# Performance work log

Measured on AMD Instinct MI355X. Metric: run time of the kernel, lower is better.

The kernel has to match this reference:

```python
import jax, jax.numpy as jnp
import numpy as np

EPS = 1e-5
GROUPS = 8
NUM_HEADS = 8


def setup_inputs() -> dict:
    key = jax.random.key(0)
    ks = jax.random.split(key, 6)
    C = 512
    s = 1.0 / np.sqrt(C)
    return {
        "x": jax.random.normal(ks[0], (8, C, 32, 32), dtype=jnp.float32),
        "gn_w": jnp.ones((C,), jnp.float32),
        "gn_b": jnp.zeros((C,), jnp.float32),
        "wq": jax.random.normal(ks[1], (C, C), jnp.float32) * s,
        "bq": jnp.zeros((C,), jnp.float32),
        "wk": jax.random.normal(ks[2], (C, C), jnp.float32) * s,
        "bk": jnp.zeros((C,), jnp.float32),
        "wv": jax.random.normal(ks[3], (C, C), jnp.float32) * s,
        "bv": jnp.zeros((C,), jnp.float32),
        "wp": jax.random.normal(ks[4], (C, C), jnp.float32) * s,
        "bp": jnp.zeros((C,), jnp.float32),
    }


def _group_norm(x, w, b):
    # x: [B, C, H, W]; normalize per group over (C//G, H, W)
    B, C, H, W = x.shape
    xg = x.reshape(B, GROUPS, -1)
    mean = xg.mean(axis=-1, keepdims=True)
    var = xg.var(axis=-1, keepdims=True)
    xn = ((xg - mean) * jax.lax.rsqrt(var + EPS)).reshape(B, C, H, W)
    return xn * w[None, :, None, None] + b[None, :, None, None]


def reference(x, gn_w, gn_b, wq, bq, wk, bk, wv, bv, wp, bp):
    B, C, H, W = x.shape
    n_heads = NUM_HEADS
    d = C // n_heads
    scale = 1.0 / np.sqrt(d)

    x_flat = x.reshape(B, C, H * W).transpose(0, 2, 1)       # [B, S, C]
    xn = _group_norm(x, gn_w, gn_b).reshape(B, C, H * W).transpose(0, 2, 1)

    # torch Linear: y = x @ W.T + b
    q = (xn @ wq.T + bq).reshape(B, H * W, n_heads, d)        # [B, S, h, d]
    k = (xn @ wk.T + bk).reshape(B, H * W, n_heads, d)
    v = (xn @ wv.T + bv).reshape(B, H * W, n_heads, d)

    attn = jnp.einsum("bnhd,bmhd->bhnm", q, k) * scale       # [B, h, S, S]
    attn = jax.nn.softmax(attn, axis=-1)
    out = jnp.einsum("bhnm,bmhd->bnhd", attn, v).reshape(B, H * W, C)
    out = out @ wp.T + bp
    out = out + x_flat
    return out.transpose(0, 2, 1).reshape(B, C, H, W)
```

## Files before the change

### kernel.cpp

```cpp
#include <hip/hip_runtime.h>
#include <stdint.h>

typedef unsigned short u16;
using bf16x8 = __attribute__((ext_vector_type(8))) short;
using f32x4  = __attribute__((ext_vector_type(4))) float;
using f32x16 = __attribute__((ext_vector_type(16))) float;
typedef unsigned int uv2 __attribute__((ext_vector_type(2)));

#define EPS_GN 1e-5f
#define SCL 0.18033688011112042f

__device__ __forceinline__ u16 f2bf(float f) {
  union { float f; uint32_t u; } x; x.f = f;
  uint32_t r = x.u + 0x7FFFu + ((x.u >> 16) & 1u);
  return (u16)(r >> 16);
}

__device__ __forceinline__ void gload_lds16(const void* g, void* l) {
  __builtin_amdgcn_global_load_lds(
      (const __attribute__((address_space(1))) unsigned int*)g,
      (__attribute__((address_space(3))) unsigned int*)l, 16, 0, 0);
}

__device__ __forceinline__ void fence_tile() {
  asm volatile("s_waitcnt vmcnt(0)" ::: "memory");
  __builtin_amdgcn_s_barrier();
  __builtin_amdgcn_sched_barrier(0);
}

__global__ __launch_bounds__(256) void prep(const float* __restrict__ x,
    float* __restrict__ part,
    const float4* __restrict__ wq, const float4* __restrict__ wk,
    const float4* __restrict__ wv, const float4* __restrict__ wp,
    const float* __restrict__ bq, const float* __restrict__ bk,
    const float* __restrict__ bv,
    u16* __restrict__ wqkv, u16* __restrict__ wpb, float* __restrict__ bqkv) {
  if (blockIdx.x < 512) {
    int bg = blockIdx.x >> 3, seg = blockIdx.x & 7;
    const float4* base = (const float4*)(x + (size_t)bg * 65536 + (size_t)seg * 8192);
    float s = 0.f, s2 = 0.f;
    for (int i = threadIdx.x; i < 2048; i += 256) {
      float4 v = base[i];
      s  += v.x + v.y + v.z + v.w;
      s2 += v.x*v.x + v.y*v.y + v.z*v.z + v.w*v.w;
    }
    for (int m = 1; m < 64; m <<= 1) { s += __shfl_xor(s, m); s2 += __shfl_xor(s2, m); }
    __shared__ float red[4][2];
    int wave = threadIdx.x >> 6;
    if ((threadIdx.x & 63) == 0) { red[wave][0] = s; red[wave][1] = s2; }
    __syncthreads();
    if (threadIdx.x == 0) {
      float a = 0.f, b = 0.f;
      for (int w = 0; w < 4; ++w) { a += red[w][0]; b += red[w][1]; }
      part[blockIdx.x * 2] = a; part[blockIdx.x * 2 + 1] = b;
    }
  } else {
    int i = (blockIdx.x - 512) * 256 + threadIdx.x;
    int seg = i >> 16, j = i & 65535;
    const float4* w = (seg == 0) ? wq : (seg == 1) ? wk : (seg == 2) ? wv : wp;
    u16* o = (seg < 3) ? (wqkv + seg * 262144) : wpb;
    float sc = (seg == 0) ? SCL : 1.f;
    float4 v = w[j];
    o[j*4+0] = f2bf(v.x*sc); o[j*4+1] = f2bf(v.y*sc);
    o[j*4+2] = f2bf(v.z*sc); o[j*4+3] = f2bf(v.w*sc);
    if (i < 1536) bqkv[i] = (i < 512) ? bq[i]*SCL : (i < 1024) ? bk[i-512] : bv[i-1024];
  }
}

__global__ __launch_bounds__(256) void gn_apply(const float* __restrict__ x,
    const float* __restrict__ part, const float* __restrict__ w,
    const float* __restrict__ bb, u16* __restrict__ xn) {
  __shared__ float t[32][33];
  int s0 = blockIdx.x * 32, c0 = blockIdx.y * 32, b = blockIdx.z;
  int g = c0 >> 6;
  float s = 0.f, s2 = 0.f;
  for (int q = 0; q < 8; ++q) {
    s  += part[((b*8+g)*8 + q)*2];
    s2 += part[((b*8+g)*8 + q)*2 + 1];
  }
  float mean = s * (1.f/65536.f);
  float rstd = rsqrtf(s2 * (1.f/65536.f) - mean*mean + EPS_GN);
  for (int i = 0; i < 4; ++i) {
    int c = c0 + threadIdx.y + i * 8;
    float v = x[((size_t)b*512 + c)*1024 + s0 + threadIdx.x];
    t[threadIdx.y + i*8][threadIdx.x] = (v - mean) * rstd * w[c] + bb[c];
  }
  __syncthreads();
  for (int i = 0; i < 4; ++i) {
    int sdx = s0 + threadIdx.y + i * 8;
    xn[((size_t)b*1024 + sdx)*512 + c0 + threadIdx.x] = f2bf(t[threadIdx.x][threadIdx.y + i*8]);
  }
}

__global__ __launch_bounds__(256) void qkv_gemm(const u16* __restrict__ X,
    const u16* __restrict__ W, const float* __restrict__ bias,
    u16* __restrict__ qb, u16* __restrict__ kP, u16* __restrict__ vP) {
  __shared__ __align__(16) u16 As[2*64*64];
  __shared__ __align__(16) u16 Bs[2*128*64];
  const int K = 512;
  int m0 = (blockIdx.x & 127) * 64, n0 = (blockIdx.x >> 7) * 128;
  int t = threadIdx.x, lane = t & 63, wave = t >> 6;
  int wm = wave >> 1, wn = wave & 1;
  int lr = lane & 15, lg = lane >> 4;
  f32x4 acc[2][4] = {};

  auto stage = [&](int k0, int bufi) {
    u16* Ab = As + bufi * 4096;
    u16* Bb = Bs + bufi * 8192;
#pragma unroll
    for (int c = 0; c < 2; ++c) {
      int chunk = wave * 2 + c;
      int e = chunk * 512 + lane * 8;
      int r = e >> 6, col = e & 63;
      int scol = col ^ ((r & 7) << 3);
      gload_lds16(X + (size_t)(m0 + r) * K + k0 + scol, (char*)Ab + chunk * 1024);
    }
#pragma unroll
    for (int c = 0; c < 4; ++c) {
      int chunk = wave * 4 + c;
      int e = chunk * 512 + lane * 8;
      int r = e >> 6, col = e & 63;
      int scol = col ^ ((r & 7) << 3);
      gload_lds16(W + (size_t)(n0 + r) * K + k0 + scol, (char*)Bb + chunk * 1024);
    }
  };

  stage(0, 0);
  fence_tile();
  int buf = 0;
  for (int k0 = 0; k0 < K; k0 += 64) {
    if (k0 + 64 < K) stage(k0 + 64, buf ^ 1);
    const char* Ab = (const char*)(As + buf * 4096);
    const char* Bb = (const char*)(Bs + buf * 8192);
    bf16x8 af[2][2], bfr[4][2];
#pragma unroll
    for (int kk = 0; kk < 2; ++kk) {
      int ca = kk * 64 + lg * 16;
#pragma unroll
      for (int i = 0; i < 2; ++i) {
        int ra = wm * 32 + i * 16 + lr;
        af[i][kk] = *(const bf16x8*)(Ab + ((ra * 128 + ca) ^ ((ra & 7) << 4)));
      }
#pragma unroll
      for (int j = 0; j < 4; ++j) {
        int rb = wn * 64 + j * 16 + lr;
        bfr[j][kk] = *(const bf16x8*)(Bb + ((rb * 128 + ca) ^ ((rb & 7) << 4)));
      }
    }
    __builtin_amdgcn_s_setprio(1);
#pragma unroll
    for (int kk = 0; kk < 2; ++kk)
#pragma unroll
      for (int i = 0; i < 2; ++i)
#pragma unroll
        for (int j = 0; j < 4; ++j)
          acc[i][j] = __builtin_amdgcn_mfma_f32_16x16x32_bf16(af[i][kk], bfr[j][kk], acc[i][j], 0, 0, 0);
    __builtin_amdgcn_s_setprio(0);
    fence_tile();
    buf ^= 1;
  }
  if (n0 < 512) {
    for (int i = 0; i < 2; ++i)
      for (int j = 0; j < 4; ++j) {
        int col = n0 + wn * 64 + j * 16 + lr;
        float bv = bias[col];
        int rowb = m0 + wm * 32 + i * 16 + lg * 4;
        for (int r = 0; r < 4; ++r)
          qb[(size_t)(rowb + r) * 512 + col] = f2bf(acc[i][j][r] + bv);
      }
  } else if (n0 < 1024) {
    for (int i = 0; i < 2; ++i)
      for (int j = 0; j < 4; ++j) {
        int col = n0 + wn * 64 + j * 16 + lr;
        float bv = bias[col];
        int colK = col - 512;
        int h = colK >> 6, dcol = colK & 63;
        int s = dcol >> 4, hi2 = (dcol >> 3) & 1, jj = dcol & 7;
        int rowb = m0 + wm * 32 + i * 16 + lg * 4;
        int bb2 = rowb >> 10, s_in = rowb & 1023;
        int tile = s_in >> 6, kvl = s_in & 63;
        int n2 = kvl >> 5, lq0 = kvl & 31;
        size_t base = ((size_t)(((h * 8 + bb2) * 16 + tile) * 8 + n2 * 4 + s)) * 512 + jj;
        for (int r = 0; r < 4; ++r)
          kP[base + (size_t)(hi2 * 32 + lq0 + r) * 8] = f2bf(acc[i][j][r] + bv);
      }
  } else {
    for (int i = 0; i < 2; ++i)
      for (int j = 0; j < 4; ++j) {
        int col = n0 + wn * 64 + j * 16 + lr;
        float bv = bias[col];
        int rowb = m0 + wm * 32 + i * 16 + lg * 4;
        int colV = col - 1024;
        int h  = colV >> 6, dl = colV & 63;
        int dt = dl >> 5,  lqv = dl & 31;
        int bb2 = rowb >> 10, s_in = rowb & 1023;
        int tile = s_in >> 6, kvl = s_in & 63;
        int cg = kvl >> 4, hiv = (kvl >> 3) & 1, j0 = kvl & 7;
        int ii = dt * 4 + cg, lv = hiv * 32 + lqv;
        size_t u16off = ((size_t)((h * 8 + bb2) * 16 + tile)) * 4096 + (ii * 64 + lv) * 8 + j0;
        unsigned p0, p1;
        float v0 = acc[i][j][0] + bv, v1 = acc[i][j][1] + bv;
        float v2 = acc[i][j][2] + bv, v3 = acc[i][j][3] + bv;
        asm("v_cvt_pk_bf16_f32 %0, %1, %2" : "=v"(p0) : "v"(v0), "v"(v1));
        asm("v_cvt_pk_bf16_f32 %0, %1, %2" : "=v"(p1) : "v"(v2), "v"(v3));
        uint2 pk; pk.x = p0; pk.y = p1;
        *(uint2*)(vP + u16off) = pk;
      }
  }
}

__global__ __launch_bounds__(256) void proj_gemm(const u16* __restrict__ Wt,
    const u16* __restrict__ X, const float* __restrict__ bias,
    const float* __restrict__ resid, float* __restrict__ Out) {
  __shared__ __align__(16) u16 As[2*128*64];
  __shared__ __align__(16) u16 Bs[2*64*64];
  const int K = 512;
  int m0 = blockIdx.x * 64, n0 = blockIdx.y * 128;
  int t = threadIdx.x, lane = t & 63, wave = t >> 6;
  int wm = wave >> 1, wn = wave & 1;
  int lr = lane & 15, lg = lane >> 4;
  f32x4 acc[4][2] = {};

  auto stage = [&](int k0, int bufi) {
    u16* Ab = As + bufi * 8192;
    u16* Bb = Bs + bufi * 4096;
#pragma unroll
    for (int c = 0; c < 4; ++c) {
      int chunk = wave * 4 + c;
      int e = chunk * 512 + lane * 8;
      int r = e >> 6, col = e & 63;
      int scol = col ^ ((r & 7) << 3);
      gload_lds16(Wt + (size_t)(n0 + r) * K + k0 + scol, (char*)Ab + chunk * 1024);
    }
#pragma unroll
    for (int c = 0; c < 2; ++c) {
      int chunk = wave * 2 + c;
      int e = chunk * 512 + lane * 8;
      int r = e >> 6, col = e & 63;
      int scol = col ^ ((r & 7) << 3);
      gload_lds16(X + (size_t)(m0 + r) * K + k0 + scol, (char*)Bb + chunk * 1024);
    }
  };

  stage(0, 0);
  fence_tile();
  int buf = 0;
  for (int k0 = 0; k0 < K; k0 += 64) {
    if (k0 + 64 < K) stage(k0 + 64, buf ^ 1);
    const char* Ab = (const char*)(As + buf * 8192);
    const char* Bb = (const char*)(Bs + buf * 4096);
    bf16x8 af[4][2], bfr[2][2];
#pragma unroll
    for (int kk = 0; kk < 2; ++kk) {
      int ca = kk * 64 + lg * 16;
#pragma unroll
      for (int i = 0; i < 4; ++i) {
        int ra = wm * 64 + i * 16 + lr;
        af[i][kk] = *(const bf16x8*)(Ab + ((ra * 128 + ca) ^ ((ra & 7) << 4)));
      }
#pragma unroll
      for (int j = 0; j < 2; ++j) {
        int rb = wn * 32 + j * 16 + lr;
        bfr[j][kk] = *(const bf16x8*)(Bb + ((rb * 128 + ca) ^ ((rb & 7) << 4)));
      }
    }
    __builtin_amdgcn_s_setprio(1);
#pragma unroll
    for (int kk = 0; kk < 2; ++kk)
#pragma unroll
      for (int i = 0; i < 4; ++i)
#pragma unroll
        for (int j = 0; j < 2; ++j)
          acc[i][j] = __builtin_amdgcn_mfma_f32_16x16x32_bf16(af[i][kk], bfr[j][kk], acc[i][j], 0, 0, 0);
    __builtin_amdgcn_s_setprio(0);
    fence_tile();
    buf ^= 1;
  }
  for (int i = 0; i < 4; ++i)
    for (int j = 0; j < 2; ++j) {
      int mcol = m0 + wn * 32 + j * 16 + lr;
      for (int r = 0; r < 4; ++r) {
        int nrow = n0 + wm * 64 + i * 16 + lg * 4 + r;
        float v = acc[i][j][r] + bias[nrow];
        size_t b = (size_t)(mcol >> 10); int s = mcol & 1023;
        size_t addr = (b * 512 + nrow) * 1024 + s;
        Out[addr] = v + resid[addr];
      }
    }
}

__global__ __launch_bounds__(512, 4) void attn_fwd(const u16* __restrict__ qb,
    const u16* __restrict__ kP, const u16* __restrict__ vP, u16* __restrict__ o) {
  __shared__ __align__(16) u16 smem[26624];
  int bh = blockIdx.x, qb_i = blockIdx.y;
  int b = bh >> 3, h = bh & 7;
  int t = threadIdx.x, lane = t & 63, wave = t >> 6;
  int half = wave >> 2, wq4 = wave & 3;
  int lq = lane & 31, hi = lane >> 5;
  int qrow0 = qb_i * 128 + wq4 * 32;
  const u16* qp = qb + (size_t)(b * 1024 + qrow0 + lq) * 512 + h * 64 + hi * 8;
  bf16x8 qf[4];
#pragma unroll
  for (int s = 0; s < 4; ++s) qf[s] = *(const bf16x8*)(qp + s * 16);
  float li = 0.f;
  f32x16 ot[2] = {};
  const u16* kb = kP + ((size_t)((h * 8 + b) * 16 + half * 8)) * 4096 + (size_t)lane * 8;
  const u16* vb = vP + ((size_t)((h * 8 + b) * 16 + half * 8)) * 4096 + (size_t)lane * 8;

  for (int ti = 0; ti < 8; ++ti) {
    bf16x8 kf[8];
#pragma unroll
    for (int f = 0; f < 8; ++f) kf[f] = *(const bf16x8*)(kb + ti * 4096 + f * 512);
    f32x16 st[2];
#pragma unroll
    for (int n2 = 0; n2 < 2; ++n2) {
      f32x16 z = {};
      __builtin_amdgcn_s_setprio(1);
#pragma unroll
      for (int s = 0; s < 4; ++s)
        z = __builtin_amdgcn_mfma_f32_32x32x16_bf16(kf[n2 * 4 + s], qf[s], z, 0, 0, 0);
      __builtin_amdgcn_s_setprio(0);
      st[n2] = z;
    }
    float sm[16];
#pragma unroll
    for (int r = 0; r < 16; ++r) {
      float e0 = __builtin_amdgcn_exp2f(st[0][r]);
      float e1 = __builtin_amdgcn_exp2f(st[1][r]);
      st[0][r] = e0; st[1][r] = e1;
      sm[r] = e0 + e1;
    }
#pragma unroll
    for (int s = 8; s > 0; s >>= 1)
#pragma unroll
      for (int r = 0; r < s; ++r) sm[r] += sm[r + s];
    li += sm[0] + __shfl_xor(sm[0], 32);
    bf16x8 fr[4];
#pragma unroll
    for (int n2 = 0; n2 < 2; ++n2) {
#pragma unroll
      for (int c = 0; c < 2; ++c) {
        unsigned W0, W1, W2, W3;
        asm("v_cvt_pk_bf16_f32 %0, %1, %2" : "=v"(W0) : "v"(st[n2][8*c+0]), "v"(st[n2][8*c+1]));
        asm("v_cvt_pk_bf16_f32 %0, %1, %2" : "=v"(W1) : "v"(st[n2][8*c+2]), "v"(st[n2][8*c+3]));
        asm("v_cvt_pk_bf16_f32 %0, %1, %2" : "=v"(W2) : "v"(st[n2][8*c+4]), "v"(st[n2][8*c+5]));
        asm("v_cvt_pk_bf16_f32 %0, %1, %2" : "=v"(W3) : "v"(st[n2][8*c+6]), "v"(st[n2][8*c+7]));
        uv2 r02 = __builtin_amdgcn_permlane32_swap(W0, W2, false, false);
        uv2 r13 = __builtin_amdgcn_permlane32_swap(W1, W3, false, false);
        union { unsigned u[4]; bf16x8 v; } f;
        f.u[0] = r02[0]; f.u[1] = r13[0]; f.u[2] = r02[1]; f.u[3] = r13[1];
        fr[n2 * 2 + c] = f.v;
      }
    }
    bf16x8 vr[8];
#pragma unroll
    for (int i = 0; i < 8; ++i) vr[i] = *(const bf16x8*)(vb + ti * 4096 + i * 512);
    __builtin_amdgcn_s_setprio(1);
#pragma unroll
    for (int cg = 0; cg < 4; ++cg)
#pragma unroll
      for (int dt = 0; dt < 2; ++dt)
        ot[dt] = __builtin_amdgcn_mfma_f32_32x32x16_bf16(vr[dt * 4 + cg], fr[cg], ot[dt], 0, 0, 0);
    __builtin_amdgcn_s_setprio(0);
  }
  float* cbuf = (float*)smem;
  float* wreg = cbuf + wq4 * 2176;
  if (half == 0) {
#pragma unroll
    for (int dt = 0; dt < 2; ++dt)
#pragma unroll
      for (int r = 0; r < 16; ++r)
        wreg[(dt * 16 + r) * 64 + lane] = ot[dt][r];
    wreg[2048 + lane] = li;
  }
  __syncthreads();
  if (half == 1) {
    float inv = 1.f / (wreg[2048 + lane] + li);
    u16* wb = smem + 18432 + wq4 * 2048;
#pragma unroll
    for (int dt = 0; dt < 2; ++dt)
#pragma unroll
      for (int g = 0; g < 4; ++g) {
        float v0 = (wreg[(dt*16 + 4*g+0)*64 + lane] + ot[dt][4*g+0]) * inv;
        float v1 = (wreg[(dt*16 + 4*g+1)*64 + lane] + ot[dt][4*g+1]) * inv;
        float v2 = (wreg[(dt*16 + 4*g+2)*64 + lane] + ot[dt][4*g+2]) * inv;
        float v3 = (wreg[(dt*16 + 4*g+3)*64 + lane] + ot[dt][4*g+3]) * inv;
        unsigned p0, p1;
        asm("v_cvt_pk_bf16_f32 %0, %1, %2" : "=v"(p0) : "v"(v0), "v"(v1));
        asm("v_cvt_pk_bf16_f32 %0, %1, %2" : "=v"(p1) : "v"(v2), "v"(v3));
        int ch = dt * 8 + 2 * g + hi;
        int pos = ch ^ ((lq & 7) << 1);
        uint2 wv; wv.x = p0; wv.y = p1;
        *(uint2*)((char*)wb + lq * 128 + pos * 8) = wv;
      }
    int q2 = lane >> 1, j0 = lane & 1;
#pragma unroll
    for (int jj = 0; jj < 4; ++jj) {
      int j = j0 + jj * 2;
      uint4 val = *(const uint4*)((const char*)wb + q2 * 128 + ((j ^ (q2 & 7)) << 4));
      *(uint4*)(o + (size_t)(b * 1024 + qrow0 + q2) * 512 + h * 64 + j * 8) = val;
    }
  }
}

extern "C" void kernel_launch(void* const* d_in, const int* in_sizes, int n_in,
                              void* d_out, int out_size, void* d_ws, size_t ws_size,
                              hipStream_t stream) {
  const float* x    = (const float*)d_in[0];
  const float* gn_w = (const float*)d_in[1];
  const float* gn_b = (const float*)d_in[2];
  const float* wq   = (const float*)d_in[3];
  const float* bq   = (const float*)d_in[4];
  const float* wk   = (const float*)d_in[5];
  const float* bk   = (const float*)d_in[6];
  const float* wv   = (const float*)d_in[7];
  const float* bv   = (const float*)d_in[8];
  const float* wp   = (const float*)d_in[9];
  const float* bp   = (const float*)d_in[10];

  char* ws = (char*)d_ws;
  float* part  = (float*)ws;
  float* bqkv  = (float*)(ws + 4096);
  u16* wqkv = (u16*)(ws + 16384);
  u16* wpb  = (u16*)(ws + 1589248);
  u16* xn   = (u16*)(ws + 2113536);
  u16* qb   = (u16*)(ws + 10502144);
  u16* kPb  = qb + 4194304;
  u16* vPb  = (u16*)(ws + 27279360);
  u16* attno = xn;

  prep<<<1536, 256, 0, stream>>>(x, part,
      (const float4*)wq, (const float4*)wk, (const float4*)wv, (const float4*)wp,
      bq, bk, bv, wqkv, wpb, bqkv);
  gn_apply<<<dim3(32, 16, 8), dim3(32, 8), 0, stream>>>(x, part, gn_w, gn_b, xn);
  qkv_gemm<<<1536, 256, 0, stream>>>(xn, wqkv, bqkv, qb, kPb, vPb);
  attn_fwd<<<dim3(64, 8), 512, 0, stream>>>(qb, kPb, vPb, attno);
  proj_gemm<<<dim3(128, 4), 256, 0, stream>>>(wpb, attno, bp, x, (float*)d_out);
}
```

Measured before the change: 74.34 us.

## Process two query row groups per wave in attention and double-buffer K fragments

Each wave now handles 64 query rows (two 32-row groups), so every K and V fragment loaded from memory feeds twice as many MFMAs, and the grid halves along the query axis. K fragments for the next tile are prefetched into a second register set while the current tile is computed, and the V loads are issued earlier to hide latency. This raises register pressure, so launch bounds drop to 2 blocks per SM. The cross-half combine is done once per query group with extra barriers. Fewer blocks and lower occupancy may leave CUs underused.

```diff
diff --git a/kernel.cpp b/kernel.cpp
--- a/kernel.cpp
+++ b/kernel.cpp
@@ -289,116 +289,175 @@
     }
 }
 
-__global__ __launch_bounds__(512, 4) void attn_fwd(const u16* __restrict__ qb,
+__global__ __launch_bounds__(512, 2) void attn_fwd(const u16* __restrict__ qbuf,
     const u16* __restrict__ kP, const u16* __restrict__ vP, u16* __restrict__ o) {
-  __shared__ __align__(16) u16 smem[26624];
-  int bh = blockIdx.x, qb_i = blockIdx.y;
+  __shared__ float comb[4][2112];
+  __shared__ __align__(16) u16 wbuf[4][2048];
+  int bh = blockIdx.x, qb2 = blockIdx.y;
   int b = bh >> 3, h = bh & 7;
   int t = threadIdx.x, lane = t & 63, wave = t >> 6;
   int half = wave >> 2, wq4 = wave & 3;
   int lq = lane & 31, hi = lane >> 5;
-  int qrow0 = qb_i * 128 + wq4 * 32;
-  const u16* qp = qb + (size_t)(b * 1024 + qrow0 + lq) * 512 + h * 64 + hi * 8;
-  bf16x8 qf[4];
-#pragma unroll
-  for (int s = 0; s < 4; ++s) qf[s] = *(const bf16x8*)(qp + s * 16);
-  float li = 0.f;
-  f32x16 ot[2] = {};
+  int qrow0 = qb2 * 256 + wq4 * 64;
+  bf16x8 qf[2][4];
+#pragma unroll
+  for (int g = 0; g < 2; ++g) {
+    const u16* qp = qbuf + (size_t)(b * 1024 + qrow0 + g * 32 + lq) * 512 + h * 64 + hi * 8;
+#pragma unroll
+    for (int s = 0; s < 4; ++s) qf[g][s] = *(const bf16x8*)(qp + s * 16);
+  }
+  float liA = 0.f, liB = 0.f;
+  f32x16 otA0 = {}, otA1 = {}, otB0 = {}, otB1 = {};
   const u16* kb = kP + ((size_t)((h * 8 + b) * 16 + half * 8)) * 4096 + (size_t)lane * 8;
   const u16* vb = vP + ((size_t)((h * 8 + b) * 16 + half * 8)) * 4096 + (size_t)lane * 8;
 
-  for (int ti = 0; ti < 8; ++ti) {
-    bf16x8 kf[8];
-#pragma unroll
-    for (int f = 0; f < 8; ++f) kf[f] = *(const bf16x8*)(kb + ti * 4096 + f * 512);
-    f32x16 st[2];
+  bf16x8 kfA[8], kfB[8];
+#pragma unroll
+  for (int f = 0; f < 8; ++f) kfA[f] = *(const bf16x8*)(kb + f * 512);
+
+  auto tile_body = [&](int ti, bf16x8 (&kf)[8], bf16x8 (&kn)[8]) {
+    f32x16 stA[2];
 #pragma unroll
     for (int n2 = 0; n2 < 2; ++n2) {
       f32x16 z = {};
       __builtin_amdgcn_s_setprio(1);
 #pragma unroll
       for (int s = 0; s < 4; ++s)
-        z = __builtin_amdgcn_mfma_f32_32x32x16_bf16(kf[n2 * 4 + s], qf[s], z, 0, 0, 0);
+        z = __builtin_amdgcn_mfma_f32_32x32x16_bf16(kf[n2 * 4 + s], qf[0][s], z, 0, 0, 0);
       __builtin_amdgcn_s_setprio(0);
-      st[n2] = z;
-    }
-    float sm[16];
+      stA[n2] = z;
+    }
+    bf16x8 vr[8];
+#pragma unroll
+    for (int i = 0; i < 8; ++i) vr[i] = *(const bf16x8*)(vb + ti * 4096 + i * 512);
+    f32x16 stB[2];
+#pragma unroll
+    for (int n2 = 0; n2 < 2; ++n2) {
+      f32x16 z = {};
+      __builtin_amdgcn_s_setprio(1);
+#pragma unroll
+      for (int s = 0; s < 4; ++s)
+        z = __builtin_amdgcn_mfma_f32_32x32x16_bf16(kf[n2 * 4 + s], qf[1][s], z, 0, 0, 0);
+      __builtin_amdgcn_s_setprio(0);
+      stB[n2] = z;
+    }
 #pragma unroll
     for (int r = 0; r < 16; ++r) {
-      float e0 = __builtin_amdgcn_exp2f(st[0][r]);
-      float e1 = __builtin_amdgcn_exp2f(st[1][r]);
-      st[0][r] = e0; st[1][r] = e1;
-      sm[r] = e0 + e1;
-    }
-#pragma unroll
-    for (int s = 8; s > 0; s >>= 1)
-#pragma unroll
-      for (int r = 0; r < s; ++r) sm[r] += sm[r + s];
-    li += sm[0] + __shfl_xor(sm[0], 32);
-    bf16x8 fr[4];
-#pragma unroll
-    for (int n2 = 0; n2 < 2; ++n2) {
+      stA[0][r] = __builtin_amdgcn_exp2f(stA[0][r]);
+      stA[1][r] = __builtin_amdgcn_exp2f(stA[1][r]);
+      stB[0][r] = __builtin_amdgcn_exp2f(stB[0][r]);
+      stB[1][r] = __builtin_amdgcn_exp2f(stB[1][r]);
+    }
+    bf16x8 frA[4], frB[4];
+#pragma unroll
+    for (int n2 = 0; n2 < 2; ++n2)
 #pragma unroll
       for (int c = 0; c < 2; ++c) {
         unsigned W0, W1, W2, W3;
-        asm("v_cvt_pk_bf16_f32 %0, %1, %2" : "=v"(W0) : "v"(st[n2][8*c+0]), "v"(st[n2][8*c+1]));
-        asm("v_cvt_pk_bf16_f32 %0, %1, %2" : "=v"(W1) : "v"(st[n2][8*c+2]), "v"(st[n2][8*c+3]));
-        asm("v_cvt_pk_bf16_f32 %0, %1, %2" : "=v"(W2) : "v"(st[n2][8*c+4]), "v"(st[n2][8*c+5]));
-        asm("v_cvt_pk_bf16_f32 %0, %1, %2" : "=v"(W3) : "v"(st[n2][8*c+6]), "v"(st[n2][8*c+7]));
+        asm("v_cvt_pk_bf16_f32 %0, %1, %2" : "=v"(W0) : "v"(stA[n2][8*c+0]), "v"(stA[n2][8*c+1]));
+        asm("v_cvt_pk_bf16_f32 %0, %1, %2" : "=v"(W1) : "v"(stA[n2][8*c+2]), "v"(stA[n2][8*c+3]));
+        asm("v_cvt_pk_bf16_f32 %0, %1, %2" : "=v"(W2) : "v"(stA[n2][8*c+4]), "v"(stA[n2][8*c+5]));
+        asm("v_cvt_pk_bf16_f32 %0, %1, %2" : "=v"(W3) : "v"(stA[n2][8*c+6]), "v"(stA[n2][8*c+7]));
         uv2 r02 = __builtin_amdgcn_permlane32_swap(W0, W2, false, false);
         uv2 r13 = __builtin_amdgcn_permlane32_swap(W1, W3, false, false);
         union { unsigned u[4]; bf16x8 v; } f;
         f.u[0] = r02[0]; f.u[1] = r13[0]; f.u[2] = r02[1]; f.u[3] = r13[1];
-        fr[n2 * 2 + c] = f.v;
-      }
-    }
-    bf16x8 vr[8];
-#pragma unroll
-    for (int i = 0; i < 8; ++i) vr[i] = *(const bf16x8*)(vb + ti * 4096 + i * 512);
+        frA[n2 * 2 + c] = f.v;
+      }
+#pragma unroll
+    for (int n2 = 0; n2 < 2; ++n2)
+#pragma unroll
+      for (int c = 0; c < 2; ++c) {
+        unsigned W0, W1, W2, W3;
+        asm("v_cvt_pk_bf16_f32 %0, %1, %2" : "=v"(W0) : "v"(stB[n2][8*c+0]), "v"(stB[n2][8*c+1]));
+        asm("v_cvt_pk_bf16_f32 %0, %1, %2" : "=v"(W1) : "v"(stB[n2][8*c+2]), "v"(stB[n2][8*c+3]));
+        asm("v_cvt_pk_bf16_f32 %0, %1, %2" : "=v"(W2) : "v"(stB[n2][8*c+4]), "v"(stB[n2][8*c+5]));
+        asm("v_cvt_pk_bf16_f32 %0, %1, %2" : "=v"(W3) : "v"(stB[n2][8*c+6]), "v"(stB[n2][8*c+7]));
+        uv2 r02 = __builtin_amdgcn_permlane32_swap(W0, W2, false, false);
+        uv2 r13 = __builtin_amdgcn_permlane32_swap(W1, W3, false, false);
+        union { unsigned u[4]; bf16x8 v; } f;
+        f.u[0] = r02[0]; f.u[1] = r13[0]; f.u[2] = r02[1]; f.u[3] = r13[1];
+        frB[n2 * 2 + c] = f.v;
+      }
+    if (ti < 7) {
+#pragma unroll
+      for (int f = 0; f < 8; ++f) kn[f] = *(const bf16x8*)(kb + (ti + 1) * 4096 + f * 512);
+    }
+#pragma unroll
+    for (int r = 0; r < 16; ++r) { stA[0][r] += stA[1][r]; stB[0][r] += stB[1][r]; }
+#pragma unroll
+    for (int s = 8; s > 0; s >>= 1)
+#pragma unroll
+      for (int r = 0; r < s; ++r) { stA[0][r] += stA[0][r + s]; stB[0][r] += stB[0][r + s]; }
+    liA += stA[0][0];
+    liB += stB[0][0];
     __builtin_amdgcn_s_setprio(1);
 #pragma unroll
-    for (int cg = 0; cg < 4; ++cg)
-#pragma unroll
-      for (int dt = 0; dt < 2; ++dt)
-        ot[dt] = __builtin_amdgcn_mfma_f32_32x32x16_bf16(vr[dt * 4 + cg], fr[cg], ot[dt], 0, 0, 0);
+    for (int cg = 0; cg < 4; ++cg) {
+      otA0 = __builtin_amdgcn_mfma_f32_32x32x16_bf16(vr[cg],     frA[cg], otA0, 0, 0, 0);
+      otA1 = __builtin_amdgcn_mfma_f32_32x32x16_bf16(vr[4 + cg], frA[cg], otA1, 0, 0, 0);
+    }
+#pragma unroll
+    for (int cg = 0; cg < 4; ++cg) {
+      otB0 = __builtin_amdgcn_mfma_f32_32x32x16_bf16(vr[cg],     frB[cg], otB0, 0, 0, 0);
+      otB1 = __builtin_amdgcn_mfma_f32_32x32x16_bf16(vr[4 + cg], frB[cg], otB1, 0, 0, 0);
+    }
     __builtin_amdgcn_s_setprio(0);
-  }
-  float* cbuf = (float*)smem;
-  float* wreg = cbuf + wq4 * 2176;
-  if (half == 0) {
-#pragma unroll
-    for (int dt = 0; dt < 2; ++dt)
-#pragma unroll
-      for (int r = 0; r < 16; ++r)
-        wreg[(dt * 16 + r) * 64 + lane] = ot[dt][r];
-    wreg[2048 + lane] = li;
-  }
-  __syncthreads();
-  if (half == 1) {
-    float inv = 1.f / (wreg[2048 + lane] + li);
-    u16* wb = smem + 18432 + wq4 * 2048;
-#pragma unroll
-    for (int dt = 0; dt < 2; ++dt)
-#pragma unroll
-      for (int g = 0; g < 4; ++g) {
-        float v0 = (wreg[(dt*16 + 4*g+0)*64 + lane] + ot[dt][4*g+0]) * inv;
-        float v1 = (wreg[(dt*16 + 4*g+1)*64 + lane] + ot[dt][4*g+1]) * inv;
-        float v2 = (wreg[(dt*16 + 4*g+2)*64 + lane] + ot[dt][4*g+2]) * inv;
-        float v3 = (wreg[(dt*16 + 4*g+3)*64 + lane] + ot[dt][4*g+3]) * inv;
-        unsigned p0, p1;
-        asm("v_cvt_pk_bf16_f32 %0, %1, %2" : "=v"(p0) : "v"(v0), "v"(v1));
-        asm("v_cvt_pk_bf16_f32 %0, %1, %2" : "=v"(p1) : "v"(v2), "v"(v3));
-        int ch = dt * 8 + 2 * g + hi;
-        int pos = ch ^ ((lq & 7) << 1);
-        uint2 wv; wv.x = p0; wv.y = p1;
-        *(uint2*)((char*)wb + lq * 128 + pos * 8) = wv;
-      }
-    int q2 = lane >> 1, j0 = lane & 1;
-#pragma unroll
-    for (int jj = 0; jj < 4; ++jj) {
-      int j = j0 + jj * 2;
-      uint4 val = *(const uint4*)((const char*)wb + q2 * 128 + ((j ^ (q2 & 7)) << 4));
-      *(uint4*)(o + (size_t)(b * 1024 + qrow0 + q2) * 512 + h * 64 + j * 8) = val;
+  };
+
+#pragma unroll
+  for (int p = 0; p < 4; ++p) {
+    tile_body(p * 2,     kfA, kfB);
+    tile_body(p * 2 + 1, kfB, kfA);
+  }
+
+  float liAa = liA + __shfl_xor(liA, 32);
+  float liBa = liB + __shfl_xor(liB, 32);
+
+  float* wreg = comb[wq4];
+#pragma unroll
+  for (int g = 0; g < 2; ++g) {
+    f32x16 o0 = g ? otB0 : otA0;
+    f32x16 o1 = g ? otB1 : otA1;
+    float lig = g ? liBa : liAa;
+    __syncthreads();
+    if (half == 0) {
+#pragma unroll
+      for (int r = 0; r < 16; ++r) {
+        wreg[r * 64 + lane]         = o0[r];
+        wreg[(16 + r) * 64 + lane]  = o1[r];
+      }
+      wreg[2048 + lane] = lig;
+    }
+    __syncthreads();
+    if (half == 1) {
+      float inv = 1.f / (wreg[2048 + lane] + lig);
+      u16* wb = wbuf[wq4];
+#pragma unroll
+      for (int dt = 0; dt < 2; ++dt) {
+        f32x16 oo = dt ? o1 : o0;
+#pragma unroll
+        for (int gg = 0; gg < 4; ++gg) {
+          float v0 = (wreg[(dt*16 + 4*gg+0)*64 + lane] + oo[4*gg+0]) * inv;
+          float v1 = (wreg[(dt*16 + 4*gg+1)*64 + lane] + oo[4*gg+1]) * inv;
+          float v2 = (wreg[(dt*16 + 4*gg+2)*64 + lane] + oo[4*gg+2]) * inv;
+          float v3 = (wreg[(dt*16 + 4*gg+3)*64 + lane] + oo[4*gg+3]) * inv;
+          unsigned p0, p1;
+          asm("v_cvt_pk_bf16_f32 %0, %1, %2" : "=v"(p0) : "v"(v0), "v"(v1));
+          asm("v_cvt_pk_bf16_f32 %0, %1, %2" : "=v"(p1) : "v"(v2), "v"(v3));
+          int ch = dt * 8 + 2 * gg + hi;
+          int pos = ch ^ ((lq & 7) << 1);
+          uint2 wv; wv.x = p0; wv.y = p1;
+          *(uint2*)((char*)wb + lq * 128 + pos * 8) = wv;
+        }
+      }
+      int q2 = lane >> 1, j0 = lane & 1;
+#pragma unroll
+      for (int jj = 0; jj < 4; ++jj) {
+        int j = j0 + jj * 2;
+        uint4 val = *(const uint4*)((const char*)wb + q2 * 128 + ((j ^ (q2 & 7)) << 4));
+        *(uint4*)(o + (size_t)(b * 1024 + qrow0 + g * 32 + q2) * 512 + h * 64 + j * 8) = val;
+      }
     }
   }
 }
@@ -434,6 +493,6 @@
       bq, bk, bv, wqkv, wpb, bqkv);
   gn_apply<<<dim3(32, 16, 8), dim3(32, 8), 0, stream>>>(x, part, gn_w, gn_b, xn);
   qkv_gemm<<<1536, 256, 0, stream>>>(xn, wqkv, bqkv, qb, kPb, vPb);
-  attn_fwd<<<dim3(64, 8), 512, 0, stream>>>(qb, kPb, vPb, attno);
+  attn_fwd<<<dim3(64, 4), 512, 0, stream>>>(qb, kPb, vPb, attno);
   proj_gemm<<<dim3(128, 4), 256, 0, stream>>>(wpb, attno, bp, x, (float*)d_out);
 }
```

After: 91.71 us. 1.23x slower.
